# Kernel optimization log

Hardware: AMD Instinct MI355X
Metric: run time of the kernel (lower is better)

The kernel has to match this reference:

```python
import jax, jax.numpy as jnp
import numpy as np

# Dimensions from init_kwargs
B, C, H, W = 128, 3, 64, 64
K, S, P = 5, 2, 2            # kernel, stride, padding
OC = 64                      # base_channels
OH = (H + 2 * P - K) // S + 1  # 32
OW = (W + 2 * P - K) // S + 1  # 32
FC_IN = OC * OH * OW         # 65536
HID = 24 * OC                # 1536
NCLS = 10
EPS = 1e-5                   # BatchNorm eps (torch default)


def setup_inputs() -> dict:
    key = jax.random.key(0)
    ks = jax.random.split(key, 4)
    x = jax.random.normal(ks[0], (B, C, H, W), dtype=jnp.float32)
    # LocallyConnected2d: unshared weight per output location [OC, C*K*K, OH, OW]
    lc_w = jax.random.normal(ks[1], (OC, C * K * K, OH, OW), dtype=jnp.float32) * 0.05
    bn1_g = jnp.ones((OC,), jnp.float32)
    bn1_b = jnp.zeros((OC,), jnp.float32)
    fc1_w = jax.random.normal(ks[2], (HID, FC_IN), dtype=jnp.float32) * 0.01
    bn2_g = jnp.ones((HID,), jnp.float32)
    bn2_b = jnp.zeros((HID,), jnp.float32)
    fc2_w = jax.random.normal(ks[3], (NCLS, HID), dtype=jnp.float32) * 0.02
    return {"x": x, "lc_w": lc_w, "bn1_g": bn1_g, "bn1_b": bn1_b,
            "fc1_w": fc1_w, "bn2_g": bn2_g, "bn2_b": bn2_b, "fc2_w": fc2_w}


def reference(x, lc_w, bn1_g, bn1_b, fc1_w, bn2_g, bn2_b, fc2_w):
    # --- LocallyConnected2d (no bias): unfold + per-location contraction ---
    # patches: [B, C*K*K, OH, OW]
    patches = jax.lax.conv_general_dilated_patches(
        x, filter_shape=(K, K), window_strides=(S, S),
        padding=((P, P), (P, P)))
    out = jnp.einsum('bphw,ophw->bohw', patches, lc_w)  # [B, OC, OH, OW]

    # --- BatchNorm2d (training mode: batch stats, biased var) + ReLU ---
    mean = out.mean(axis=(0, 2, 3))
    var = out.var(axis=(0, 2, 3))
    out = (out - mean[None, :, None, None]) * jax.lax.rsqrt(var + EPS)[None, :, None, None]
    out = out * bn1_g[None, :, None, None] + bn1_b[None, :, None, None]
    out = jax.nn.relu(out)

    # --- Classifier: Linear -> BN1d -> ReLU -> Linear ---
    h = out.reshape(B, -1) @ fc1_w.T  # [B, HID]
    m2 = h.mean(axis=0)
    v2 = h.var(axis=0)
    h = (h - m2) * jax.lax.rsqrt(v2 + EPS) * bn2_g + bn2_b
    h = jax.nn.relu(h)
    return h @ fc2_w.T  # [B, NCLS]
```

## Files before the change

### kernel.cpp

```cpp
#include <hip/hip_runtime.h>
#include <hip/hip_bf16.h>
#include <stdint.h>

#define B_   128
#define C_   3
#define H_   64
#define W_   64
#define KS   5
#define OC   64
#define OH   32
#define OW   32
#define PSZ  75
#define FCIN 65536
#define HID  1536
#define NCLS 10
#define EPSV 1e-5f

typedef __attribute__((ext_vector_type(8))) short  bf16x8;
typedef __attribute__((ext_vector_type(8))) short  short8;
typedef __attribute__((ext_vector_type(4))) float  f32x4;

static __device__ __forceinline__ float bf2f(short u) {
  union { unsigned int i; float f; } v;
  v.i = ((unsigned int)(unsigned short)u) << 16;
  return v.f;
}
static __device__ __forceinline__ short f2bf(float f) {
  union { float f; unsigned int i; } v; v.f = f;
  unsigned int r = v.i + 0x7FFF + ((v.i >> 16) & 1);
  return (short)(r >> 16);
}

static __device__ __forceinline__ void gld16(const unsigned short* g, unsigned short* l) {
  __builtin_amdgcn_global_load_lds(
      (const __attribute__((address_space(1))) unsigned int*)g,
      (__attribute__((address_space(3))) unsigned int*)l, 16, 0, 0);
}
static __device__ __forceinline__ void gld16f(const float* g, float* l) {
  __builtin_amdgcn_global_load_lds(
      (const __attribute__((address_space(1))) unsigned int*)g,
      (__attribute__((address_space(3))) unsigned int*)l, 16, 0, 0);
}

__global__ __launch_bounds__(256, 2) void k1_conv(
    const float* __restrict__ x, const float* __restrict__ lcw,
    unsigned short* __restrict__ outb) {
  const int h  = blockIdx.x;
  const int og = blockIdx.y;
  const int zb = blockIdx.z;
  const int tid = threadIdx.x;
  const int w  = tid & 31;
  const int ot = tid >> 5;
  const int oc = og * 8 + ot;

  __shared__ float xs[16][C_][KS][68];

  float wr[PSZ];
  {
    const float* wp = lcw + (long)oc * PSZ * 1024 + h * 32 + w;
    #pragma unroll
    for (int p = 0; p < PSZ; ++p) wr[p] = wp[(long)p * 1024];
  }

  const int row0 = 2 * h - 2;
  for (int g = 0; g < 2; ++g) {
    const int bg = zb * 2 + g;
    if (g) __syncthreads();

    if (tid < 240) {
      int t = tid;
      int r = t % KS;  t /= KS;
      int c = t % C_;
      int b = t / C_;
      xs[b][c][r][0] = 0.f; xs[b][c][r][1] = 0.f;
      xs[b][c][r][66] = 0.f; xs[b][c][r][67] = 0.f;
    }
    for (int v = tid; v < 16 * C_ * KS * 16; v += 256) {
      int col4 = v & 15;
      int t    = v >> 4;
      int r    = t % KS;  t /= KS;
      int c    = t % C_;
      int b    = t / C_;
      int grow = row0 + r;
      f32x4 val = (f32x4){0.f, 0.f, 0.f, 0.f};
      if ((unsigned)grow < 64u)
        val = *(const f32x4*)&x[(((long)(bg * 16 + b) * C_ + c) * 64 + grow) * 64 + col4 * 4];
      *(f32x4*)&xs[b][c][r][2 + col4 * 4] = val;
    }
    __syncthreads();

    float acc[16];
    #pragma unroll
    for (int b = 0; b < 16; ++b) acc[b] = 0.f;

    #pragma unroll
    for (int c = 0; c < C_; ++c)
      #pragma unroll
      for (int kh = 0; kh < KS; ++kh)
        #pragma unroll
        for (int kw = 0; kw < KS; ++kw) {
          const float wv = wr[(c * KS + kh) * KS + kw];
          const int col = 2 * w + kw;
          #pragma unroll
          for (int b = 0; b < 16; ++b)
            acc[b] += wv * xs[b][c][kh][col];
        }

    #pragma unroll
    for (int b = 0; b < 16; ++b)
      outb[((long)(bg * 16 + b) * OC + oc) * 1024 + h * 32 + w] =
          (unsigned short)f2bf(acc[b]);
  }
}

__global__ __launch_bounds__(1024) void k2_stats(
    const unsigned short* __restrict__ outb,
    const float* __restrict__ g, const float* __restrict__ bta,
    float* __restrict__ sc, float* __restrict__ sh) {
  const int o = blockIdx.x;
  const int tid = threadIdx.x;
  float s = 0.f, s2 = 0.f;
  const int i8 = (tid & 127) * 8;
  const int bsub = tid >> 7;
  for (int pass = 0; pass < 16; ++pass) {
    int b = bsub + pass * 8;
    const short8 v = *(const short8*)(outb + (((long)b * OC + o) << 10) + i8);
    #pragma unroll
    for (int j = 0; j < 8; ++j) { float f = bf2f(v[j]); s += f; s2 += f * f; }
  }
  #pragma unroll
  for (int off = 32; off; off >>= 1) {
    s  += __shfl_down(s, off);
    s2 += __shfl_down(s2, off);
  }
  __shared__ float ls[16], ls2[16];
  int wid = tid >> 6;
  if ((tid & 63) == 0) { ls[wid] = s; ls2[wid] = s2; }
  __syncthreads();
  if (tid == 0) {
    float ts = 0.f, ts2 = 0.f;
    for (int i = 0; i < 16; ++i) { ts += ls[i]; ts2 += ls2[i]; }
    const float inv = 1.0f / (float)(B_ * 1024);
    float mean = ts * inv;
    float var  = ts2 * inv - mean * mean;
    float rstd = 1.0f / sqrtf(var + EPSV);
    float scv  = g[o] * rstd;
    sc[o] = scv;
    sh[o] = bta[o] - mean * scv;
  }
}

__global__ __launch_bounds__(256) void k25_pack(
    const unsigned short* __restrict__ outb,
    const float* __restrict__ sc, const float* __restrict__ sh,
    unsigned short* __restrict__ ab) {
  const int c = blockIdx.x * 256 + threadIdx.x;
  const int l15 = c & 15;
  const int lq  = (c >> 4) & 3;
  const int mf  = (c >> 6) & 7;
  const int kb  = c >> 9;
  const int m   = mf * 16 + l15;
  const int k   = kb * 32 + lq * 8;
  const int o   = k >> 10;
  const int hw  = k & 1023;
  float scv = sc[o], shv = sh[o];
  short8 v = *(const short8*)(outb + ((long)m * 64 + o) * 1024 + hw);
  short8 r;
  #pragma unroll
  for (int j = 0; j < 8; ++j) {
    float f = bf2f(v[j]) * scv + shv;
    r[j] = f2bf(fmaxf(f, 0.f));
  }
  *(short8*)(ab + (long)c * 8) = r;
}

__global__ __launch_bounds__(256, 3) void k3_gemm(
    const unsigned short* __restrict__ ab, const float* __restrict__ w1,
    float* __restrict__ part, int ksteps, int splits) {
  const int nwg = 24 * splits;
  const int chunk = nwg >> 3;
  const int bid = blockIdx.x;
  const int lid = (bid & 7) * chunk + (bid >> 3);
  const int split = lid / 24;
  const int ntile = lid % 24;

  const int tid  = threadIdx.x;
  const int lane = tid & 63;
  const int wid  = tid >> 6;
  const int n0   = ntile * 64 + wid * 16;
  const int l15  = lane & 15;
  const int lq   = lane >> 4;

  __shared__ unsigned short sa[3][4096];
  __shared__ float sw[3][4][512];

  const int kb0 = split * ksteps;
  const int kmask = ksteps - 1;
  const int phase = (lid * 29) & kmask;
  const long wsrc = (long)(n0 + l15) * FCIN + (long)kb0 * 32 + lq * 8;
  const int last = ksteps - 1;

#define STAGE(T, BUF) do {                                                   \
    int Tp = ((T) + phase) & kmask;                                          \
    long gb = ((long)(kb0 + Tp) * 512 + wid * 128) * 8;                      \
    unsigned short* lb = &sa[BUF][wid * 1024];                               \
    gld16(ab + gb + (long)lane * 8, lb);                                     \
    gld16(ab + gb + 512 + (long)lane * 8, lb + 512);                         \
    const float* wg = w1 + wsrc + (long)Tp * 32;                             \
    float* wlb = &sw[BUF][wid][0];                                           \
    gld16f(wg, wlb);                                                         \
    gld16f(wg + 4, wlb + 256);                                               \
  } while (0)

#define COMPUTE(X) do {                                                      \
    f32x4 wv0 = *(const f32x4*)&sw[X][wid][lane * 4];                        \
    f32x4 wv1 = *(const f32x4*)&sw[X][wid][256 + lane * 4];                  \
    bf16x8 bfr;                                                              \
    _Pragma("unroll")                                                        \
    for (int j = 0; j < 4; ++j) bfr[j] = f2bf(wv0[j]);                       \
    _Pragma("unroll")                                                        \
    for (int j = 0; j < 4; ++j) bfr[4 + j] = f2bf(wv1[j]);                   \
    __builtin_amdgcn_s_setprio(1);                                           \
    _Pragma("unroll")                                                        \
    for (int m = 0; m < 8; ++m) {                                            \
      bf16x8 afr = *(const bf16x8*)(&sa[X][m * 512 + lane * 8]);             \
      acc[m] = __builtin_amdgcn_mfma_f32_16x16x32_bf16(afr, bfr, acc[m], 0, 0, 0); \
    }                                                                        \
    __builtin_amdgcn_s_setprio(0);                                           \
  } while (0)

  f32x4 acc[8];
  #pragma unroll
  for (int m = 0; m < 8; ++m) acc[m] = (f32x4){0.f, 0.f, 0.f, 0.f};

  STAGE(0, 0);
  STAGE((1 <= last ? 1 : last), 1);

  for (int t = 0; t < ksteps; ++t) {
    asm volatile("s_waitcnt vmcnt(4)" ::: "memory");
    __builtin_amdgcn_sched_barrier(0);
    __builtin_amdgcn_s_barrier();
    __builtin_amdgcn_sched_barrier(0);
    int tn = (t + 2 <= last) ? (t + 2) : last;
    STAGE(tn, (t + 2) % 3);
    COMPUTE(t % 3);
  }
#undef STAGE
#undef COMPUTE

  float* pp = part + (long)split * (B_ * HID);
  #pragma unroll
  for (int m = 0; m < 8; ++m) {
    int row = m * 16 + lq * 4;
    #pragma unroll
    for (int r = 0; r < 4; ++r)
      pp[(long)(row + r) * HID + n0 + l15] = acc[m][r];
  }
}

__global__ __launch_bounds__(256) void k4_bn2(
    const float* __restrict__ part, const float* __restrict__ g2,
    const float* __restrict__ b2, float* __restrict__ h2, int splits) {
  const int nb = blockIdx.x;
  const int tid = threadIdx.x;
  const int nl = tid & 3;
  const int bt = tid >> 2;
  const int n  = nb * 4 + nl;

  float h0 = 0.f, h1 = 0.f;
  for (int s = 0; s < splits; ++s) {
    const float* pp = part + (long)s * (B_ * HID) + n;
    h0 += pp[(long)bt * HID];
    h1 += pp[(long)(bt + 64) * HID];
  }
  float s1 = h0 + h1, s2v = h0 * h0 + h1 * h1;

  __shared__ float r1[256], r2[256];
  r1[tid] = s1; r2[tid] = s2v;
  __syncthreads();
  for (int off = 32; off; off >>= 1) {
    if (bt < off) { r1[tid] += r1[tid + off * 4]; r2[tid] += r2[tid + off * 4]; }
    __syncthreads();
  }
  __shared__ float scs[4], shs[4];
  if (bt == 0) {
    float mean = r1[nl] * (1.0f / 128.f);
    float var  = r2[nl] * (1.0f / 128.f) - mean * mean;
    float rstd = 1.0f / sqrtf(var + EPSV);
    float sc = g2[n] * rstd;
    scs[nl] = sc; shs[nl] = b2[n] - mean * sc;
  }
  __syncthreads();
  float sc = scs[nl], shf = shs[nl];
  h2[(long)bt * HID + n]        = fmaxf(h0 * sc + shf, 0.f);
  h2[(long)(bt + 64) * HID + n] = fmaxf(h1 * sc + shf, 0.f);
}

__global__ __launch_bounds__(256) void k5_fc2(
    const float* __restrict__ h2, const float* __restrict__ w2,
    float* __restrict__ out) {
  const int b = blockIdx.x;
  const int tid = threadIdx.x;
  float acc[NCLS];
  #pragma unroll
  for (int c = 0; c < NCLS; ++c) acc[c] = 0.f;
  for (int n = tid; n < HID; n += 256) {
    float hvv = h2[(long)b * HID + n];
    #pragma unroll
    for (int c = 0; c < NCLS; ++c) acc[c] += hvv * w2[c * HID + n];
  }
  #pragma unroll
  for (int off = 32; off; off >>= 1)
    #pragma unroll
    for (int c = 0; c < NCLS; ++c) acc[c] += __shfl_down(acc[c], off);
  __shared__ float ls[4][NCLS];
  int wid = tid >> 6;
  if ((tid & 63) == 0)
    for (int c = 0; c < NCLS; ++c) ls[wid][c] = acc[c];
  __syncthreads();
  if (tid < NCLS)
    out[b * NCLS + tid] = ls[0][tid] + ls[1][tid] + ls[2][tid] + ls[3][tid];
}

extern "C" void kernel_launch(void* const* d_in, const int* in_sizes, int n_in,
                              void* d_out, int out_size, void* d_ws, size_t ws_size,
                              hipStream_t stream) {
  const float* x    = (const float*)d_in[0];
  const float* lcw  = (const float*)d_in[1];
  const float* bn1g = (const float*)d_in[2];
  const float* bn1b = (const float*)d_in[3];
  const float* fc1w = (const float*)d_in[4];
  const float* bn2g = (const float*)d_in[5];
  const float* bn2b = (const float*)d_in[6];
  const float* fc2w = (const float*)d_in[7];
  float* out = (float*)d_out;

  char* ws = (char*)d_ws;
  unsigned short* outb = (unsigned short*)(ws);
  unsigned short* ab   = (unsigned short*)(ws + (size_t)16 * 1024 * 1024);
  float* sc1 = (float*)(ws + (size_t)32 * 1024 * 1024);
  float* sh1 = sc1 + 64;
  size_t base = (size_t)32 * 1024 * 1024 + 4096;
  float* part = (float*)(ws + base);

  int splits = 32;
  size_t h2need = (size_t)B_ * HID * 4;
  while (splits > 4 && base + (size_t)splits * B_ * HID * 4 + h2need > ws_size)
    splits >>= 1;
  float* h2 = (float*)(ws + base + (size_t)splits * B_ * HID * 4);

  k1_conv<<<dim3(32, 8, 4), 256, 0, stream>>>(x, lcw, outb);
  k2_stats<<<64, 1024, 0, stream>>>(outb, bn1g, bn1b, sc1, sh1);
  k25_pack<<<4096, 256, 0, stream>>>(outb, sc1, sh1, ab);
  int ksteps = FCIN / splits / 32;
  k3_gemm<<<24 * splits, 256, 0, stream>>>(ab, fc1w, part, ksteps, splits);
  k4_bn2<<<384, 256, 0, stream>>>(part, bn2g, bn2b, h2, splits);
  k5_fc2<<<128, 256, 0, stream>>>(h2, fc2w, out);
}
```

Baseline: 228.5 us.

## Deepen GEMM prefetch pipeline and restructure conv to two channels per thread

The fc1 GEMM now keeps five LDS stages in flight instead of three, so four loads run ahead of compute, and occupancy is lowered to two workgroups per CU to fit the larger buffers. The goal is to hide more global-memory latency on the bandwidth-bound weight stream. The locally connected conv now stores its input tile in LDS as bf16 and makes each thread compute two output channels, loading weights one input channel at a time to relieve register pressure. This halves the conv grid but rounds the input to bf16, which adds error and per-element unpacking work.

Result: slower. 400.3 us (+75.2%).

```diff
diff --git a/kernel.cpp b/kernel.cpp
--- a/kernel.cpp
+++ b/kernel.cpp
@@ -30,6 +30,9 @@
   unsigned int r = v.i + 0x7FFF + ((v.i >> 16) & 1);
   return (short)(r >> 16);
 }
+static __device__ __forceinline__ float u2f(unsigned int u) {
+  union { unsigned int i; float f; } v; v.i = u; return v.f;
+}
 
 static __device__ __forceinline__ void gld16(const unsigned short* g, unsigned short* l) {
   __builtin_amdgcn_global_load_lds(
@@ -51,16 +54,9 @@
   const int tid = threadIdx.x;
   const int w  = tid & 31;
   const int ot = tid >> 5;
-  const int oc = og * 8 + ot;
-
-  __shared__ float xs[16][C_][KS][68];
-
-  float wr[PSZ];
-  {
-    const float* wp = lcw + (long)oc * PSZ * 1024 + h * 32 + w;
-    #pragma unroll
-    for (int p = 0; p < PSZ; ++p) wr[p] = wp[(long)p * 1024];
-  }
+  const int o0 = og * 16 + ot * 2;
+
+  __shared__ unsigned short xs[16][C_][KS][72];
 
   const int row0 = 2 * h - 2;
   for (int g = 0; g < 2; ++g) {
@@ -72,8 +68,10 @@
       int r = t % KS;  t /= KS;
       int c = t % C_;
       int b = t / C_;
-      xs[b][c][r][0] = 0.f; xs[b][c][r][1] = 0.f;
-      xs[b][c][r][66] = 0.f; xs[b][c][r][67] = 0.f;
+      *(unsigned int*)&xs[b][c][r][0]  = 0u;
+      *(unsigned int*)&xs[b][c][r][66] = 0u;
+      *(unsigned int*)&xs[b][c][r][68] = 0u;
+      *(unsigned int*)&xs[b][c][r][70] = 0u;
     }
     for (int v = tid; v < 16 * C_ * KS * 16; v += 256) {
       int col4 = v & 15;
@@ -85,31 +83,58 @@
       f32x4 val = (f32x4){0.f, 0.f, 0.f, 0.f};
       if ((unsigned)grow < 64u)
         val = *(const f32x4*)&x[(((long)(bg * 16 + b) * C_ + c) * 64 + grow) * 64 + col4 * 4];
-      *(f32x4*)&xs[b][c][r][2 + col4 * 4] = val;
+      unsigned int p0 = ((unsigned int)(unsigned short)f2bf(val[0])) |
+                        (((unsigned int)(unsigned short)f2bf(val[1])) << 16);
+      unsigned int p1 = ((unsigned int)(unsigned short)f2bf(val[2])) |
+                        (((unsigned int)(unsigned short)f2bf(val[3])) << 16);
+      *(unsigned int*)&xs[b][c][r][2 + col4 * 4]     = p0;
+      *(unsigned int*)&xs[b][c][r][2 + col4 * 4 + 2] = p1;
     }
     __syncthreads();
 
-    float acc[16];
-    #pragma unroll
-    for (int b = 0; b < 16; ++b) acc[b] = 0.f;
-
-    #pragma unroll
-    for (int c = 0; c < C_; ++c)
+    float acc[2][16];
+    #pragma unroll
+    for (int oo = 0; oo < 2; ++oo)
       #pragma unroll
-      for (int kh = 0; kh < KS; ++kh)
+      for (int b = 0; b < 16; ++b) acc[oo][b] = 0.f;
+
+    for (int c = 0; c < C_; ++c) {
+      float wr2[2][25];
+      {
+        const float* wpA = lcw + ((long)o0 * PSZ + c * 25) * 1024 + h * 32 + w;
+        const float* wpB = lcw + ((long)(o0 + 1) * PSZ + c * 25) * 1024 + h * 32 + w;
         #pragma unroll
-        for (int kw = 0; kw < KS; ++kw) {
-          const float wv = wr[(c * KS + kh) * KS + kw];
-          const int col = 2 * w + kw;
-          #pragma unroll
-          for (int b = 0; b < 16; ++b)
-            acc[b] += wv * xs[b][c][kh][col];
+        for (int p = 0; p < 25; ++p) {
+          wr2[0][p] = wpA[(long)p * 1024];
+          wr2[1][p] = wpB[(long)p * 1024];
         }
-
-    #pragma unroll
-    for (int b = 0; b < 16; ++b)
-      outb[((long)(bg * 16 + b) * OC + oc) * 1024 + h * 32 + w] =
-          (unsigned short)f2bf(acc[b]);
+      }
+      #pragma unroll
+      for (int kh = 0; kh < KS; ++kh) {
+        #pragma unroll
+        for (int b = 0; b < 16; ++b) {
+          const unsigned int* rowp = (const unsigned int*)&xs[b][c][kh][0];
+          unsigned int d0 = rowp[w];
+          unsigned int d1 = rowp[w + 1];
+          unsigned int d2 = rowp[w + 2];
+          float v0 = u2f(d0 << 16), v1 = u2f(d0 & 0xffff0000u);
+          float v2 = u2f(d1 << 16), v3 = u2f(d1 & 0xffff0000u);
+          float v4 = u2f(d2 << 16);
+          const int pb = kh * 5;
+          acc[0][b] += wr2[0][pb] * v0 + wr2[0][pb + 1] * v1 + wr2[0][pb + 2] * v2
+                     + wr2[0][pb + 3] * v3 + wr2[0][pb + 4] * v4;
+          acc[1][b] += wr2[1][pb] * v0 + wr2[1][pb + 1] * v1 + wr2[1][pb + 2] * v2
+                     + wr2[1][pb + 3] * v3 + wr2[1][pb + 4] * v4;
+        }
+      }
+    }
+
+    #pragma unroll
+    for (int oo = 0; oo < 2; ++oo)
+      #pragma unroll
+      for (int b = 0; b < 16; ++b)
+        outb[((long)(bg * 16 + b) * OC + (o0 + oo)) * 1024 + h * 32 + w] =
+            (unsigned short)f2bf(acc[oo][b]);
   }
 }
 
@@ -174,7 +199,7 @@
   *(short8*)(ab + (long)c * 8) = r;
 }
 
-__global__ __launch_bounds__(256, 3) void k3_gemm(
+__global__ __launch_bounds__(256, 2) void k3_gemm(
     const unsigned short* __restrict__ ab, const float* __restrict__ w1,
     float* __restrict__ part, int ksteps, int splits) {
   const int nwg = 24 * splits;
@@ -191,8 +216,8 @@
   const int l15  = lane & 15;
   const int lq   = lane >> 4;
 
-  __shared__ unsigned short sa[3][4096];
-  __shared__ float sw[3][4][512];
+  __shared__ unsigned short sa[5][4096];
+  __shared__ float sw[5][4][512];
 
   const int kb0 = split * ksteps;
   const int kmask = ksteps - 1;
@@ -234,17 +259,20 @@
   for (int m = 0; m < 8; ++m) acc[m] = (f32x4){0.f, 0.f, 0.f, 0.f};
 
   STAGE(0, 0);
-  STAGE((1 <= last ? 1 : last), 1);
+  STAGE(1, 1);
+  STAGE(2, 2);
+  STAGE(3, 3);
 
   for (int t = 0; t < ksteps; ++t) {
-    asm volatile("s_waitcnt vmcnt(4)" ::: "memory");
+    asm volatile("s_waitcnt vmcnt(12)" ::: "memory");
     __builtin_amdgcn_sched_barrier(0);
     __builtin_amdgcn_s_barrier();
     __builtin_amdgcn_sched_barrier(0);
-    int tn = (t + 2 <= last) ? (t + 2) : last;
-    STAGE(tn, (t + 2) % 3);
-    COMPUTE(t % 3);
-  }
+    int tn = (t + 4 <= last) ? (t + 4) : last;
+    STAGE(tn, (t + 4) % 5);
+    COMPUTE(t % 5);
+  }
+  asm volatile("s_waitcnt vmcnt(0)" ::: "memory");
 #undef STAGE
 #undef COMPUTE
 
@@ -349,7 +377,7 @@
     splits >>= 1;
   float* h2 = (float*)(ws + base + (size_t)splits * B_ * HID * 4);
 
-  k1_conv<<<dim3(32, 8, 4), 256, 0, stream>>>(x, lcw, outb);
+  k1_conv<<<dim3(32, 4, 4), 256, 0, stream>>>(x, lcw, outb);
   k2_stats<<<64, 1024, 0, stream>>>(outb, bn1g, bn1b, sc1, sh1);
   k25_pack<<<4096, 256, 0, stream>>>(outb, sc1, sh1, ab);
   int ksteps = FCIN / splits / 32;
```
